# Optimization experiments

Hardware: AMD Instinct MI355X
Metric: run time of the kernel (lower is better)

Reference implementation:

```python
import jax, jax.numpy as jnp
import numpy as np

D_MODEL = 1024
N_HEADS = 16
D_K = D_MODEL // N_HEADS


def setup_inputs() -> dict:
    key = jax.random.key(0)
    ks = jax.random.split(key, 9)
    B, S = 4, 2048
    scale = 1.0 / np.sqrt(D_MODEL)
    x = jax.random.normal(ks[0], (B, S, D_MODEL), dtype=jnp.float32)
    # Linear params: weight [out,in] (torch convention), bias [out]
    wq = jax.random.uniform(ks[1], (D_MODEL, D_MODEL), jnp.float32, -scale, scale)
    bq = jax.random.uniform(ks[2], (D_MODEL,), jnp.float32, -scale, scale)
    wk = jax.random.uniform(ks[3], (D_MODEL, D_MODEL), jnp.float32, -scale, scale)
    bk = jax.random.uniform(ks[4], (D_MODEL,), jnp.float32, -scale, scale)
    wv = jax.random.uniform(ks[5], (D_MODEL, D_MODEL), jnp.float32, -scale, scale)
    bv = jax.random.uniform(ks[6], (D_MODEL,), jnp.float32, -scale, scale)
    wo = jax.random.uniform(ks[7], (D_MODEL, D_MODEL), jnp.float32, -scale, scale)
    bo = jax.random.uniform(ks[8], (D_MODEL,), jnp.float32, -scale, scale)
    return {"x": x, "wq": wq, "bq": bq, "wk": wk, "bk": bk,
            "wv": wv, "bv": bv, "wo": wo, "bo": bo}


def reference(x, wq, bq, wk, bk, wv, bv, wo, bo):
    B, S, _ = x.shape
    # QKV projections (torch Linear: x @ W^T + b)
    q = x @ wq.T + bq
    k = x @ wk.T + bk
    v = x @ wv.T + bv
    # [B, H, S, D_K]
    q = q.reshape(B, S, N_HEADS, D_K).transpose(0, 2, 1, 3)
    k = k.reshape(B, S, N_HEADS, D_K).transpose(0, 2, 1, 3)
    v = v.reshape(B, S, N_HEADS, D_K).transpose(0, 2, 1, 3)
    scores = jnp.einsum('bhqd,bhkd->bhqk', q, k) / jnp.sqrt(jnp.float32(D_K))
    attn = jax.nn.softmax(scores, axis=-1)
    out = jnp.einsum('bhqk,bhkd->bhqd', attn, v)
    out = out.transpose(0, 2, 1, 3).reshape(B, S, D_MODEL)
    return out @ wo.T + bo
```

## Files before the change

### kernel.cpp

```cpp
#include <hip/hip_runtime.h>

#define DMODEL 1024
#define NHEADS 16
#define DK 64
#define BATCH 4
#define SEQ 2048
#define MROWS (BATCH * SEQ)
#define NT 16

typedef __attribute__((ext_vector_type(8))) short bf16x8;
typedef __attribute__((ext_vector_type(8))) unsigned short u16x8;
typedef __attribute__((ext_vector_type(4))) unsigned short u16x4;
typedef __attribute__((ext_vector_type(4))) float f32x4;
typedef __attribute__((ext_vector_type(16))) float f32x16;
typedef __attribute__((ext_vector_type(2))) unsigned int u32x2;
typedef __attribute__((ext_vector_type(4))) unsigned int u32x4;

using gld_gptr = const __attribute__((address_space(1))) unsigned int*;
using gld_lptr = __attribute__((address_space(3))) unsigned int*;

#define QSCALE 0.18033688011112042f

__device__ inline unsigned short f32_bf16(float f) {
    unsigned int u = __float_as_uint(f);
    u += 0x7FFFu + ((u >> 16) & 1u);
    return (unsigned short)(u >> 16);
}

__device__ inline unsigned int cvtpk_bf16(float a, float b) {
    unsigned int r;
    asm("v_cvt_pk_bf16_f32 %0, %1, %2" : "=v"(r) : "v"(a), "v"(b));
    return r;
}

__device__ inline f32x16 fz16() {
    f32x16 v;
#pragma unroll
    for (int i = 0; i < 16; ++i) v[i] = 0.f;
    return v;
}

struct Conv5 {
    const float* s[5];
    unsigned short* d[5];
};

__global__ __launch_bounds__(256) void conv5_kernel(Conv5 c) {
    int bx = blockIdx.x;
    int which, idx;
    if (bx < 4096) { which = 0; idx = bx; }
    else { which = 1 + ((bx - 4096) >> 9); idx = (bx - 4096) & 511; }
    int i = idx * 256 + threadIdx.x;
    const float4* s = (const float4*)(c.s[which] + (size_t)i * 8);
    float4 a = s[0], b = s[1];
    u16x8 o;
    o[0] = f32_bf16(a.x); o[1] = f32_bf16(a.y); o[2] = f32_bf16(a.z); o[3] = f32_bf16(a.w);
    o[4] = f32_bf16(b.x); o[5] = f32_bf16(b.y); o[6] = f32_bf16(b.z); o[7] = f32_bf16(b.w);
    *(u16x8*)(c.d[which] + (size_t)i * 8) = o;
}

__device__ __forceinline__ void stage_half(const unsigned short* mat, int row0, int step,
                                           char* lds_half, int tid) {
#pragma unroll
    for (int rnd = 0; rnd < 2; ++rnd) {
        int rl = rnd * 64 + (tid >> 3);
        int c16 = (tid & 7) ^ (rl & 7);
        const unsigned short* g = mat + (size_t)(row0 + rl) * DMODEL + step * 64 + c16 * 8;
        __builtin_amdgcn_global_load_lds((gld_gptr)g,
            (gld_lptr)(lds_half + rnd * 8192 + (tid >> 6) * 1024), 16, 0, 0);
    }
}

__device__ __forceinline__ bf16x8 lds_frag(const char* base, int row, int kk, int l) {
    int kb = kk * 64 + (l >> 4) * 16;
    return *(const bf16x8*)(base + row * 128 + (kb ^ ((row & 7) << 4)));
}

template <int QP>
__device__ __forceinline__ void phase_reads(const char* Ab, const char* Bb,
                                            bf16x8 (&breg)[4][2], bf16x8 (&areg)[2][2],
                                            int wm, int wn, int l) {
    int l15 = l & 15;
    if constexpr (QP == 0) {
#pragma unroll
        for (int nt = 0; nt < 4; ++nt)
#pragma unroll
            for (int kk = 0; kk < 2; ++kk)
                breg[nt][kk] = lds_frag(Bb, wn * 64 + nt * 16 + l15, kk, l);
    }
#pragma unroll
    for (int j = 0; j < 2; ++j)
#pragma unroll
        for (int kk = 0; kk < 2; ++kk)
            areg[j][kk] = lds_frag(Ab, wm * 128 + (QP * 2 + j) * 16 + l15, kk, l);
}

template <int QP>
__device__ __forceinline__ void phase_mfma(bf16x8 (&areg)[2][2], bf16x8 (&breg)[4][2],
                                           f32x4 (&acc)[8][4]) {
    __builtin_amdgcn_s_setprio(1);
#pragma unroll
    for (int j = 0; j < 2; ++j)
#pragma unroll
        for (int nt = 0; nt < 4; ++nt) {
            acc[QP * 2 + j][nt] = __builtin_amdgcn_mfma_f32_16x16x32_bf16(
                areg[j][0], breg[nt][0], acc[QP * 2 + j][nt], 0, 0, 0);
            acc[QP * 2 + j][nt] = __builtin_amdgcn_mfma_f32_16x16x32_bf16(
                areg[j][1], breg[nt][1], acc[QP * 2 + j][nt], 0, 0, 0);
        }
    __builtin_amdgcn_s_setprio(0);
}

#define GBAR() __builtin_amdgcn_s_barrier()
#define VMC4() asm volatile("s_waitcnt vmcnt(4)" ::: "memory")

template <bool F32OUT>
__device__ __forceinline__ void gemm_core(const unsigned short* __restrict__ Am,
                                          const unsigned short* __restrict__ Bm,
                                          const float* __restrict__ bias, void* Cv,
                                          float scl, int m0, int n0) {
    __shared__ __align__(16) char lds[131072];
    char* A0 = lds;
    char* B0 = lds + 32768;
    char* A1 = lds + 65536;
    char* B1 = lds + 98304;

    int tid = threadIdx.x, l = tid & 63, w = tid >> 6;
    int wm = w >> 2, wn = w & 3;

    f32x4 acc[8][4];
#pragma unroll
    for (int i = 0; i < 8; ++i)
#pragma unroll
        for (int j = 0; j < 4; ++j) acc[i][j] = (f32x4){0.f, 0.f, 0.f, 0.f};

    stage_half(Am, m0,       0, A0,         tid);
    stage_half(Am, m0 + 128, 0, A0 + 16384, tid);
    stage_half(Bm, n0,       0, B0,         tid);
    stage_half(Bm, n0 + 128, 0, B0 + 16384, tid);
    stage_half(Bm, n0,       1, B1,         tid);
    stage_half(Bm, n0 + 128, 1, B1 + 16384, tid);
    VMC4();
    GBAR();

    bf16x8 breg[4][2];
    for (int i = 0; i < NT / 2; ++i) {
        int E = 2 * i;
        bf16x8 areg[2][2];
        phase_reads<0>(A0, B0, breg, areg, wm, wn, l);
        stage_half(Am, m0,       (E + 1) & 15, A1, tid);
        GBAR(); phase_mfma<0>(areg, breg, acc); GBAR();

        phase_reads<1>(A0, B0, breg, areg, wm, wn, l);
        stage_half(Am, m0 + 128, (E + 1) & 15, A1 + 16384, tid);
        GBAR(); phase_mfma<1>(areg, breg, acc); GBAR();

        phase_reads<2>(A0, B0, breg, areg, wm, wn, l);
        stage_half(Bm, n0,       (E + 2) & 15, B0, tid);
        GBAR(); phase_mfma<2>(areg, breg, acc); GBAR();

        phase_reads<3>(A0, B0, breg, areg, wm, wn, l);
        stage_half(Bm, n0 + 128, (E + 2) & 15, B0 + 16384, tid);
        GBAR(); phase_mfma<3>(areg, breg, acc);
        VMC4();
        GBAR();

        phase_reads<0>(A1, B1, breg, areg, wm, wn, l);
        stage_half(Am, m0,       (E + 2) & 15, A0, tid);
        GBAR(); phase_mfma<0>(areg, breg, acc); GBAR();

        phase_reads<1>(A1, B1, breg, areg, wm, wn, l);
        stage_half(Am, m0 + 128, (E + 2) & 15, A0 + 16384, tid);
        GBAR(); phase_mfma<1>(areg, breg, acc); GBAR();

        phase_reads<2>(A1, B1, breg, areg, wm, wn, l);
        stage_half(Bm, n0,       (E + 3) & 15, B1, tid);
        GBAR(); phase_mfma<2>(areg, breg, acc); GBAR();

        phase_reads<3>(A1, B1, breg, areg, wm, wn, l);
        stage_half(Bm, n0 + 128, (E + 3) & 15, B1 + 16384, tid);
        GBAR(); phase_mfma<3>(areg, breg, acc);
        VMC4();
        GBAR();
    }

    int lm = l >> 4, ln = l & 15;
#pragma unroll
    for (int nt = 0; nt < 4; ++nt) {
        int col = n0 + wn * 64 + nt * 16 + ln;
        float bv = bias[col];
#pragma unroll
        for (int mt = 0; mt < 8; ++mt)
#pragma unroll
            for (int r = 0; r < 4; ++r) {
                int row = m0 + wm * 128 + mt * 16 + lm * 4 + r;
                float v = (acc[mt][nt][r] + bv) * scl;
                if constexpr (F32OUT)
                    ((float*)Cv)[(size_t)row * DMODEL + col] = v;
                else
                    ((unsigned short*)Cv)[(size_t)row * DMODEL + col] = f32_bf16(v);
            }
    }
}

struct QkvPtrs {
    const unsigned short* w[3];
    const float* b[3];
    unsigned short* c[3];
    float scale[3];
};

__global__ __launch_bounds__(512, 2) void gemm_qkv8(const unsigned short* __restrict__ A, QkvPtrs p) {
    int sel = blockIdx.y >> 2;
    int n0 = (blockIdx.y & 3) * 256;
    int m0 = blockIdx.x * 256;
    gemm_core<false>(A, p.w[sel], p.b[sel], p.c[sel], p.scale[sel], m0, n0);
}

__global__ __launch_bounds__(512, 2) void gemm_out8(const unsigned short* __restrict__ A,
                                                    const unsigned short* __restrict__ B,
                                                    const float* __restrict__ bias,
                                                    float* __restrict__ C) {
    gemm_core<true>(A, B, bias, C, 1.0f, blockIdx.x * 256, blockIdx.y * 256);
}

#define BUILD_PW(dst, pv, o)                                                        \
    {                                                                               \
        unsigned int wa_ = cvtpk_bf16(pv[(o) + 0], pv[(o) + 1]);                    \
        unsigned int wb_ = cvtpk_bf16(pv[(o) + 2], pv[(o) + 3]);                    \
        unsigned int wc_ = cvtpk_bf16(pv[(o) + 4], pv[(o) + 5]);                    \
        unsigned int wd_ = cvtpk_bf16(pv[(o) + 6], pv[(o) + 7]);                    \
        u32x2 ra_ = __builtin_amdgcn_permlane32_swap(wa_, wc_, false, false);       \
        u32x2 rb_ = __builtin_amdgcn_permlane32_swap(wb_, wd_, false, false);       \
        dst = (u32x4){ra_[0], rb_[0], ra_[1], rb_[1]};                              \
    }

#define ABAR() asm volatile("s_barrier" ::: "memory")
#define AVMC0() asm volatile("s_waitcnt vmcnt(0)" ::: "memory")

__device__ __forceinline__ void stage_k(const unsigned short* kp, int kt,
                                        unsigned short* kbuf, int l, int w) {
#pragma unroll
    for (int i = 0; i < 2; ++i) {
        int chunk = w + i * 4;
        int srccol = (l & 7) ^ (l >> 3);
        const unsigned short* g = kp + (size_t)(kt * 64 + chunk * 8 + (l >> 3)) * DMODEL + srccol * 8;
        __builtin_amdgcn_global_load_lds((gld_gptr)g, (gld_lptr)(kbuf + chunk * 512), 16, 0, 0);
    }
}

__device__ __forceinline__ void load_v(const unsigned short* vp, int kt, int tid,
                                       bf16x8& va, bf16x8& vb) {
    int kvp = (tid & 31) * 2;
    int d0 = (tid >> 5) * 8;
    va = *(const bf16x8*)&vp[(size_t)(kt * 64 + kvp) * DMODEL + d0];
    vb = *(const bf16x8*)&vp[(size_t)(kt * 64 + kvp + 1) * DMODEL + d0];
}

__device__ __forceinline__ void write_v(unsigned short* vbuf, int tid, bf16x8 va, bf16x8 vb) {
    int kvp = (tid & 31) * 2;
    int d0 = (tid >> 5) * 8;
#pragma unroll
    for (int j = 0; j < 8; ++j) {
        int d = d0 + j;
        unsigned int val = ((unsigned int)(unsigned short)va[j]) |
                           (((unsigned int)(unsigned short)vb[j]) << 16);
        int byt = d * 128 + (((kvp >> 3) ^ (d & 7)) << 4) + (kvp & 7) * 2;
        *(unsigned int*)((char*)vbuf + byt) = val;
    }
}

__global__ __launch_bounds__(256, 2) void attn_kernel(const unsigned short* __restrict__ Q,
                                                      const unsigned short* __restrict__ Km,
                                                      const unsigned short* __restrict__ Vm,
                                                      unsigned short* __restrict__ O) {
    __shared__ unsigned short Klds[2][64 * 64];
    __shared__ unsigned short Vt[2][64 * 64];

    int flat = blockIdx.y * gridDim.x + blockIdx.x;
    int xcd = flat & 7, idx = flat >> 3;
    int bh = xcd * 8 + (idx & 7);
    int qt = idx >> 3;
    int b = bh >> 4, h = bh & 15;
    int tid = threadIdx.x, l = tid & 63, w = tid >> 6;
    int lq = l & 31, hf = l >> 5;
    const size_t base = ((size_t)b * SEQ) * DMODEL + (size_t)h * DK;
    const unsigned short* qp = Q + base;
    const unsigned short* kp = Km + base;
    const unsigned short* vp = Vm + base;
    int q0 = qt * 256 + w * 64;

    bf16x8 qf[2][4];
#pragma unroll
    for (int sb = 0; sb < 2; ++sb)
#pragma unroll
        for (int ks = 0; ks < 4; ++ks)
            qf[sb][ks] = *(const bf16x8*)&qp[(size_t)(q0 + sb * 32 + lq) * DMODEL + ks * 16 + hf * 8];

    f32x16 accO[2][2];
    accO[0][0] = fz16(); accO[0][1] = fz16(); accO[1][0] = fz16(); accO[1][1] = fz16();
    float l_r[2] = {0.f, 0.f};

    bf16x8 va, vb;
    stage_k(kp, 0, Klds[0], l, w);
    load_v(vp, 0, tid, va, vb);
    AVMC0();
    write_v(Vt[0], tid, va, vb);
    ABAR();

    for (int kt = 0; kt < SEQ / 64; ++kt) {
        int cur = kt & 1, nxt = cur ^ 1;
        bool pre = (kt + 1 < SEQ / 64);
        if (pre) {
            stage_k(kp, kt + 1, Klds[nxt], l, w);
            load_v(vp, kt + 1, tid, va, vb);
        }

        f32x16 s[2][2];
        s[0][0] = fz16(); s[0][1] = fz16(); s[1][0] = fz16(); s[1][1] = fz16();
        __builtin_amdgcn_s_setprio(1);
#pragma unroll
        for (int ks = 0; ks < 4; ++ks) {
            int col16 = ks * 2 + hf;
            bf16x8 kf0 = *(const bf16x8*)((const char*)Klds[cur] + lq * 128 + ((col16 ^ (lq & 7)) << 4));
            bf16x8 kf1 = *(const bf16x8*)((const char*)Klds[cur] + (lq + 32) * 128 + ((col16 ^ (lq & 7)) << 4));
            s[0][0] = __builtin_amdgcn_mfma_f32_32x32x16_bf16(kf0, qf[0][ks], s[0][0], 0, 0, 0);
            s[0][1] = __builtin_amdgcn_mfma_f32_32x32x16_bf16(kf1, qf[0][ks], s[0][1], 0, 0, 0);
            s[1][0] = __builtin_amdgcn_mfma_f32_32x32x16_bf16(kf0, qf[1][ks], s[1][0], 0, 0, 0);
            s[1][1] = __builtin_amdgcn_mfma_f32_32x32x16_bf16(kf1, qf[1][ks], s[1][1], 0, 0, 0);
        }
        __builtin_amdgcn_s_setprio(0);

        u32x4 pw[2][4];
#pragma unroll
        for (int sb = 0; sb < 2; ++sb) {
            float rs = 0.f;
#pragma unroll
            for (int r = 0; r < 16; ++r) { s[sb][0][r] = __builtin_amdgcn_exp2f(s[sb][0][r]); rs += s[sb][0][r]; }
#pragma unroll
            for (int r = 0; r < 16; ++r) { s[sb][1][r] = __builtin_amdgcn_exp2f(s[sb][1][r]); rs += s[sb][1][r]; }
            rs += __shfl_xor(rs, 32);
            l_r[sb] += rs;
            BUILD_PW(pw[sb][0], s[sb][0], 0);
            BUILD_PW(pw[sb][1], s[sb][0], 8);
            BUILD_PW(pw[sb][2], s[sb][1], 0);
            BUILD_PW(pw[sb][3], s[sb][1], 8);
        }

        __builtin_amdgcn_s_setprio(1);
#pragma unroll
        for (int ks = 0; ks < 4; ++ks) {
            int col16 = ks * 2 + hf;
            int d1 = 32 + lq;
            bf16x8 vf0 = *(const bf16x8*)((const char*)Vt[cur] + lq * 128 + ((col16 ^ (lq & 7)) << 4));
            bf16x8 vf1 = *(const bf16x8*)((const char*)Vt[cur] + d1 * 128 + ((col16 ^ (d1 & 7)) << 4));
            bf16x8 pf0 = *(bf16x8*)&pw[0][ks];
            bf16x8 pf1 = *(bf16x8*)&pw[1][ks];
            accO[0][0] = __builtin_amdgcn_mfma_f32_32x32x16_bf16(vf0, pf0, accO[0][0], 0, 0, 0);
            accO[0][1] = __builtin_amdgcn_mfma_f32_32x32x16_bf16(vf1, pf0, accO[0][1], 0, 0, 0);
            accO[1][0] = __builtin_amdgcn_mfma_f32_32x32x16_bf16(vf0, pf1, accO[1][0], 0, 0, 0);
            accO[1][1] = __builtin_amdgcn_mfma_f32_32x32x16_bf16(vf1, pf1, accO[1][1], 0, 0, 0);
        }
        __builtin_amdgcn_s_setprio(0);

        if (pre) {
            AVMC0();
            write_v(Vt[nxt], tid, va, vb);
        }
        ABAR();
    }

#pragma unroll
    for (int sb = 0; sb < 2; ++sb) {
        float inv = 1.0f / l_r[sb];
        unsigned short* op = O + base + (size_t)(q0 + sb * 32 + lq) * DMODEL;
#pragma unroll
        for (int db = 0; db < 2; ++db)
#pragma unroll
            for (int rg = 0; rg < 4; ++rg) {
                int dbase = db * 32 + rg * 8 + hf * 4;
                u16x4 ov;
#pragma unroll
                for (int j = 0; j < 4; ++j) ov[j] = f32_bf16(accO[sb][db][rg * 4 + j] * inv);
                *(u16x4*)&op[dbase] = ov;
            }
    }
}

extern "C" void kernel_launch(void* const* d_in, const int* in_sizes, int n_in,
                              void* d_out, int out_size, void* d_ws, size_t ws_size,
                              hipStream_t stream) {
    (void)in_sizes; (void)n_in; (void)out_size; (void)ws_size;
    const float* x  = (const float*)d_in[0];
    const float* wq = (const float*)d_in[1];
    const float* bq = (const float*)d_in[2];
    const float* wk = (const float*)d_in[3];
    const float* bk = (const float*)d_in[4];
    const float* wv = (const float*)d_in[5];
    const float* bv = (const float*)d_in[6];
    const float* wo = (const float*)d_in[7];
    const float* bo = (const float*)d_in[8];
    float* out = (float*)d_out;
    char* ws = (char*)d_ws;

    unsigned short* xb  = (unsigned short*)(ws);
    unsigned short* wqb = (unsigned short*)(ws + (16ull << 20));
    unsigned short* wkb = (unsigned short*)(ws + (18ull << 20));
    unsigned short* wvb = (unsigned short*)(ws + (20ull << 20));
    unsigned short* wob = (unsigned short*)(ws + (22ull << 20));
    unsigned short* qb  = (unsigned short*)(ws + (24ull << 20));
    unsigned short* kb  = (unsigned short*)(ws + (40ull << 20));
    unsigned short* vb  = (unsigned short*)(ws + (56ull << 20));
    unsigned short* ob  = xb;

    Conv5 cv;
    cv.s[0] = x;  cv.d[0] = xb;
    cv.s[1] = wq; cv.d[1] = wqb;
    cv.s[2] = wk; cv.d[2] = wkb;
    cv.s[3] = wv; cv.d[3] = wvb;
    cv.s[4] = wo; cv.d[4] = wob;
    conv5_kernel<<<4096 + 4 * 512, 256, 0, stream>>>(cv);

    QkvPtrs p;
    p.w[0] = wqb; p.w[1] = wkb; p.w[2] = wvb;
    p.b[0] = bq;  p.b[1] = bk;  p.b[2] = bv;
    p.c[0] = qb;  p.c[1] = kb;  p.c[2] = vb;
    p.scale[0] = QSCALE; p.scale[1] = 1.0f; p.scale[2] = 1.0f;
    gemm_qkv8<<<dim3(32, 12), 512, 0, stream>>>(xb, p);

    attn_kernel<<<dim3(8, 64), 256, 0, stream>>>(qb, kb, vb, ob);

    gemm_out8<<<dim3(32, 4), 512, 0, stream>>>(ob, wob, bo, out);
}
```

Before: 188.9 us.

## Shrink attention blocks to two waves with 128 query rows each

Changes the attention launch from 256-thread blocks covering 256 query rows to 128-thread blocks covering 128 rows, doubling the grid. K/V staging is redistributed so each thread loads four K chunks and four V rows, and writes the transposed V as 8-byte stores. The per-row exp sum becomes a tree reduction instead of a serial chain. Smaller blocks should allow more resident blocks and better load balance, but each K/V tile is now reused by fewer query rows, so global K/V traffic doubles.

```diff
diff --git a/kernel.cpp b/kernel.cpp
--- a/kernel.cpp
+++ b/kernel.cpp
@@ -241,39 +241,41 @@
 __device__ __forceinline__ void stage_k(const unsigned short* kp, int kt,
                                         unsigned short* kbuf, int l, int w) {
 #pragma unroll
-    for (int i = 0; i < 2; ++i) {
-        int chunk = w + i * 4;
+    for (int i = 0; i < 4; ++i) {
+        int chunk = w * 4 + i;
         int srccol = (l & 7) ^ (l >> 3);
         const unsigned short* g = kp + (size_t)(kt * 64 + chunk * 8 + (l >> 3)) * DMODEL + srccol * 8;
         __builtin_amdgcn_global_load_lds((gld_gptr)g, (gld_lptr)(kbuf + chunk * 512), 16, 0, 0);
     }
 }
 
-__device__ __forceinline__ void load_v(const unsigned short* vp, int kt, int tid,
-                                       bf16x8& va, bf16x8& vb) {
-    int kvp = (tid & 31) * 2;
-    int d0 = (tid >> 5) * 8;
-    va = *(const bf16x8*)&vp[(size_t)(kt * 64 + kvp) * DMODEL + d0];
-    vb = *(const bf16x8*)&vp[(size_t)(kt * 64 + kvp + 1) * DMODEL + d0];
-}
-
-__device__ __forceinline__ void write_v(unsigned short* vbuf, int tid, bf16x8 va, bf16x8 vb) {
-    int kvp = (tid & 31) * 2;
-    int d0 = (tid >> 5) * 8;
+__device__ __forceinline__ void load_v(const unsigned short* vp, int kt, int tid, bf16x8 (&vr)[4]) {
+    int kvb = (tid & 15) * 4;
+    int d0 = (tid >> 4) * 8;
+#pragma unroll
+    for (int j = 0; j < 4; ++j)
+        vr[j] = *(const bf16x8*)&vp[(size_t)(kt * 64 + kvb + j) * DMODEL + d0];
+}
+
+__device__ __forceinline__ void write_v(unsigned short* vbuf, int tid, bf16x8 (&vr)[4]) {
+    int kvb = (tid & 15) * 4;
+    int d0 = (tid >> 4) * 8;
 #pragma unroll
     for (int j = 0; j < 8; ++j) {
         int d = d0 + j;
-        unsigned int val = ((unsigned int)(unsigned short)va[j]) |
-                           (((unsigned int)(unsigned short)vb[j]) << 16);
-        int byt = d * 128 + (((kvp >> 3) ^ (d & 7)) << 4) + (kvp & 7) * 2;
-        *(unsigned int*)((char*)vbuf + byt) = val;
-    }
-}
-
-__global__ __launch_bounds__(256, 2) void attn_kernel(const unsigned short* __restrict__ Q,
-                                                      const unsigned short* __restrict__ Km,
-                                                      const unsigned short* __restrict__ Vm,
-                                                      unsigned short* __restrict__ O) {
+        unsigned int lo = ((unsigned int)(unsigned short)vr[0][j]) |
+                          (((unsigned int)(unsigned short)vr[1][j]) << 16);
+        unsigned int hi = ((unsigned int)(unsigned short)vr[2][j]) |
+                          (((unsigned int)(unsigned short)vr[3][j]) << 16);
+        int byt = d * 128 + (((kvb >> 3) ^ (d & 7)) << 4) + (kvb & 7) * 2;
+        *(u32x2*)((char*)vbuf + byt) = (u32x2){lo, hi};
+    }
+}
+
+__global__ __launch_bounds__(128) void attn_kernel(const unsigned short* __restrict__ Q,
+                                                   const unsigned short* __restrict__ Km,
+                                                   const unsigned short* __restrict__ Vm,
+                                                   unsigned short* __restrict__ O) {
     __shared__ unsigned short Klds[2][64 * 64];
     __shared__ unsigned short Vt[2][64 * 64];
 
@@ -288,7 +290,7 @@
     const unsigned short* qp = Q + base;
     const unsigned short* kp = Km + base;
     const unsigned short* vp = Vm + base;
-    int q0 = qt * 256 + w * 64;
+    int q0 = qt * 128 + w * 64;
 
     bf16x8 qf[2][4];
 #pragma unroll
@@ -301,11 +303,11 @@
     accO[0][0] = fz16(); accO[0][1] = fz16(); accO[1][0] = fz16(); accO[1][1] = fz16();
     float l_r[2] = {0.f, 0.f};
 
-    bf16x8 va, vb;
+    bf16x8 vr[4];
     stage_k(kp, 0, Klds[0], l, w);
-    load_v(vp, 0, tid, va, vb);
+    load_v(vp, 0, tid, vr);
     AVMC0();
-    write_v(Vt[0], tid, va, vb);
+    write_v(Vt[0], tid, vr);
     ABAR();
 
     for (int kt = 0; kt < SEQ / 64; ++kt) {
@@ -313,7 +315,7 @@
         bool pre = (kt + 1 < SEQ / 64);
         if (pre) {
             stage_k(kp, kt + 1, Klds[nxt], l, w);
-            load_v(vp, kt + 1, tid, va, vb);
+            load_v(vp, kt + 1, tid, vr);
         }
 
         f32x16 s[2][2];
@@ -334,11 +336,18 @@
         u32x4 pw[2][4];
 #pragma unroll
         for (int sb = 0; sb < 2; ++sb) {
-            float rs = 0.f;
-#pragma unroll
-            for (int r = 0; r < 16; ++r) { s[sb][0][r] = __builtin_amdgcn_exp2f(s[sb][0][r]); rs += s[sb][0][r]; }
-#pragma unroll
-            for (int r = 0; r < 16; ++r) { s[sb][1][r] = __builtin_amdgcn_exp2f(s[sb][1][r]); rs += s[sb][1][r]; }
+#pragma unroll
+            for (int r = 0; r < 16; ++r) s[sb][0][r] = __builtin_amdgcn_exp2f(s[sb][0][r]);
+#pragma unroll
+            for (int r = 0; r < 16; ++r) s[sb][1][r] = __builtin_amdgcn_exp2f(s[sb][1][r]);
+            float e[8];
+#pragma unroll
+            for (int r = 0; r < 8; ++r) e[r] = s[sb][0][r] + s[sb][0][r + 8];
+#pragma unroll
+            for (int r = 0; r < 8; ++r) e[r] += s[sb][1][r] + s[sb][1][r + 8];
+#pragma unroll
+            for (int r = 0; r < 4; ++r) e[r] += e[r + 4];
+            float rs = (e[0] + e[1]) + (e[2] + e[3]);
             rs += __shfl_xor(rs, 32);
             l_r[sb] += rs;
             BUILD_PW(pw[sb][0], s[sb][0], 0);
@@ -365,7 +374,7 @@
 
         if (pre) {
             AVMC0();
-            write_v(Vt[nxt], tid, va, vb);
+            write_v(Vt[nxt], tid, vr);
         }
         ABAR();
     }
@@ -428,7 +437,7 @@
     p.scale[0] = QSCALE; p.scale[1] = 1.0f; p.scale[2] = 1.0f;
     gemm_qkv8<<<dim3(32, 12), 512, 0, stream>>>(xb, p);
 
-    attn_kernel<<<dim3(8, 64), 256, 0, stream>>>(qb, kb, vb, ob);
+    attn_kernel<<<dim3(16, 64), 128, 0, stream>>>(qb, kb, vb, ob);
 
     gemm_out8<<<dim3(32, 4), 512, 0, stream>>>(ob, wob, bo, out);
 }
```

Measured after the change: 237.9 us. +25.9%, slower.
